# Optimization experiments

Hardware: AMD Instinct MI355X
Metric: run time of the kernel (lower is better)

The kernel has to match this reference:

```python
import jax, jax.numpy as jnp
import numpy as np

B, S0, DE, DT = 32, 255, 768, 256
D = DE + DT          # graph RNN input size
H = 512              # hidden_graph == hidden_edge (required by h_prev[0] = graph_state)
T = 256              # tag_representation_dim
M = 25


def _rnn_layer(x, Wih, Whh, bih, bhh):
    """Vanilla tanh RNN layer, batch_first. x: [B,S,Din] -> [B,S,H]."""
    xW = jnp.einsum('bsd,hd->bsh', x, Wih) + bih  # big GEMM hoisted out of scan
    h0 = jnp.zeros((x.shape[0], Whh.shape[0]), x.dtype)

    def step(h, xw):
        h = jnp.tanh(xw + h @ Whh.T + bhh)
        return h, h

    _, ys = jax.lax.scan(step, h0, jnp.swapaxes(xW, 0, 1))
    return jnp.swapaxes(ys, 0, 1)


def setup_inputs() -> dict:
    key = jax.random.key(0)
    ks = iter(jax.random.split(key, 40))

    def rn(shape, s=1.0):
        return jax.random.normal(next(ks), shape, jnp.float32) * s

    w = 0.04  # ~ uniform(-1/sqrt(H), 1/sqrt(H)) scale of torch RNN init
    return {
        'input': rn((B, S0, DE)),
        'tag_embeddings': rn((B, S0, DT)),
        'mask': jnp.ones((B, S0), jnp.int32),
        'sentinel': rn((D,)),
        'g0_Wih': rn((H, D), w), 'g0_Whh': rn((H, H), w), 'g0_bih': rn((H,), w), 'g0_bhh': rn((H,), w),
        'g1_Wih': rn((H, H), w), 'g1_Whh': rn((H, H), w), 'g1_bih': rn((H,), w), 'g1_bhh': rn((H,), w),
        'e0_Wih': rn((H, 1), w), 'e0_Whh': rn((H, H), w), 'e0_bih': rn((H,), w), 'e0_bhh': rn((H,), w),
        'e1_Wih': rn((H, H), w), 'e1_Whh': rn((H, H), w), 'e1_bih': rn((H,), w), 'e1_bhh': rn((H,), w),
        'cls_W': rn((1, H), w), 'cls_b': rn((1,), w),
        'ht_W': rn((T, H), w), 'ht_b': rn((T,), w),
        'dt_W': rn((T, H), w), 'dt_b': rn((T,), w),
    }


def reference(input, tag_embeddings, mask, sentinel,
              g0_Wih, g0_Whh, g0_bih, g0_bhh,
              g1_Wih, g1_Whh, g1_bih, g1_bhh,
              e0_Wih, e0_Whh, e0_bih, e0_bhh,
              e1_Wih, e1_Whh, e1_bih, e1_bhh,
              cls_W, cls_b, ht_W, ht_b, dt_W, dt_b):
    Bq = input.shape[0]
    x = jnp.concatenate([input, tag_embeddings], axis=-1)              # [B,S0,D]
    sent = jnp.broadcast_to(sentinel[None, None, :], (Bq, 1, x.shape[-1]))
    x = jnp.concatenate([sent, x], axis=1)                             # [B,S,D]
    S = x.shape[1]
    m = jnp.concatenate([jnp.ones((Bq, 1), mask.dtype), mask], axis=1)  # sentinel mask

    # --- graph RNN (2-layer tanh RNN); zero padded outputs == pad_packed_sequence ---
    y = _rnn_layer(x, g0_Wih, g0_Whh, g0_bih, g0_bhh)
    y = _rnn_layer(y, g1_Wih, g1_Whh, g1_bih, g1_bhh)
    graph_state = y * m[..., None].astype(y.dtype)                     # [B,S,H]

    N = Bq * S
    gs = graph_state.reshape(N, -1)        # layer-0 initial hidden
    x0 = jnp.ones((N, 1), graph_state.dtype)
    h1_0 = jnp.zeros_like(gs)              # layer-1 initial hidden

    def step(carry, _):
        xe, h0, h1 = carry
        h0 = jnp.tanh(xe @ e0_Wih.T + e0_bih + h0 @ e0_Whh.T + e0_bhh)
        h1 = jnp.tanh(h0 @ e1_Wih.T + e1_bih + h1 @ e1_Whh.T + e1_bhh)
        pred = h1 @ cls_W.T + cls_b        # [N,1]
        return (pred, h0, h1), pred

    _, preds = jax.lax.scan(step, (x0, gs, h1_0), None, length=M)      # [M,N,1]
    A = jnp.concatenate([x0[:, None, :], jnp.swapaxes(preds, 0, 1)], axis=1)[..., 0]  # [N,M+1]

    # --- reshape_adj: banded GraphRNN predictions -> square adjacency logits ---
    A3 = A.reshape(Bq, S, M + 1)
    i = jnp.arange(S)[:, None]
    j = jnp.arange(S)[None, :]
    k = i - j                                # offset of node j behind node i
    valid = (k >= 0) & (k <= M)
    rows = jnp.broadcast_to(i, (S, S))
    arc = A3[:, rows, jnp.clip(k, 0, M)]     # [B,S,S]
    arc_logits = jnp.where(valid[None], arc, jnp.zeros((), arc.dtype))

    # --- tag heads (dropout is identity at eval) ---
    head_tag = jax.nn.elu(graph_state @ ht_W.T + ht_b)
    dep_tag = jax.nn.elu(graph_state @ dt_W.T + dt_b)
    return arc_logits, head_tag, dep_tag
```

## Files before the change

### kernel.cpp

```cpp
#include <hip/hip_runtime.h>
#include <math.h>

typedef unsigned int u32;
typedef unsigned short u16;
typedef unsigned long long u64;
typedef __attribute__((ext_vector_type(8))) short short8;
typedef __attribute__((ext_vector_type(4))) float f32x4;

__device__ inline float bf2f(u16 v) { return __uint_as_float(((u32)v) << 16); }
__device__ inline u16 f2bf(float f) {
  u32 u = __float_as_uint(f);
  return (u16)((u + 0x7fffu + ((u >> 16) & 1u)) >> 16);
}
__device__ inline float fast_tanh(float x) {
  x = fminf(9.0f, fmaxf(-9.0f, x));
  float e = __builtin_amdgcn_exp2f(x * 2.8853900817779268f);
  return (e - 1.0f) * __builtin_amdgcn_rcpf(e + 1.0f);
}
__device__ inline void gload16(const void* g, void* l) {
  __builtin_amdgcn_global_load_lds((const __attribute__((address_space(1))) u32*)g,
                                   (__attribute__((address_space(3))) u32*)l, 16, 0, 0);
}

__global__ void k_transw(float* __restrict__ outp, const float* __restrict__ src) {
  int idx = blockIdx.x * 256 + threadIdx.x;
  int k = idx & 511, t = idx >> 9;
  outp[(size_t)k * 512 + t] = src[(size_t)t * 512 + k];
}

__global__ void k_split(u16* __restrict__ hi, u16* __restrict__ lo,
                        const float* __restrict__ src, int n) {
  int i = blockIdx.x * 256 + threadIdx.x;
  if (i >= n) return;
  float v = src[i];
  u16 h = f2bf(v);
  hi[i] = h;
  lo[i] = f2bf(v - bf2f(h));
}

__global__ void k_concat_split(u16* __restrict__ xhi, u16* __restrict__ xlo,
                               const float* __restrict__ inp, const float* __restrict__ tag,
                               const float* __restrict__ sent) {
  int gid = blockIdx.x * 256 + threadIdx.x;
  int row = gid >> 10, c = gid & 1023;
  int b = row >> 8, s = row & 255;
  float v;
  if (s == 0) v = sent[c];
  else if (c < 768) v = inp[(size_t)(b * 255 + s - 1) * 768 + c];
  else v = tag[(size_t)(b * 255 + s - 1) * 256 + (c - 768)];
  u16 h = f2bf(v);
  xhi[gid] = h;
  xlo[gid] = f2bf(v - bf2f(h));
}

__global__ void k_syncinit(u64* hbuf) {
  int i = blockIdx.x * 256 + threadIdx.x;
  if (i < 32768) {
    int pos = i & 1023;
    hbuf[i] = (pos < 512) ? (1ull << 32) : 0ull;
  }
}

__global__ __launch_bounds__(512, 1) void k_gscan_mb(
    float* __restrict__ XW, const float* __restrict__ WT,
    const int* __restrict__ mask, int layer, u64* hbuf)
{
  __shared__ float hls[528];
  const int blk = blockIdx.x;
  const int b = blk >> 2, q = blk & 3;
  const int tid = threadIdx.x;
  const int lane = tid & 63;
  const int wv = tid >> 6;
  const int colL = wv * 16 + (lane & 15);
  const int p = (lane >> 4) & 3;
  const int c = (q << 7) + colL;
  const bool fin = (p == 0);
  float wreg[128];
#pragma unroll
  for (int i = 0; i < 128; ++i)
    wreg[i] = WT[(size_t)(p * 128 + i) * 512 + c];
  u64* hb = hbuf + b * 1024;
  __syncthreads();

  for (int s = 0; s < 256; ++s) {
    float xwv = 0.f;
    size_t xwoff = 0;
    if (fin) {
      xwoff = (size_t)(b * 256 + s) * 512 + c;
      xwv = XW[xwoff];
    }
    const u32 want = (u32)(s + 1);
    u64 v;
    do {
      v = __hip_atomic_load(&hb[(s & 1) * 512 + tid], __ATOMIC_RELAXED,
                            __HIP_MEMORY_SCOPE_AGENT);
    } while ((u32)(v >> 32) < want);
    hls[(tid >> 7) * 132 + (tid & 127)] = __uint_as_float((u32)v);
    __syncthreads();
    const float* hk = &hls[p * 132];
    float a0 = 0.f, a1 = 0.f, a2 = 0.f, a3 = 0.f;
#pragma unroll
    for (int i = 0; i < 128; i += 4) {
      a0 = fmaf(wreg[i],     hk[i],     a0);
      a1 = fmaf(wreg[i + 1], hk[i + 1], a1);
      a2 = fmaf(wreg[i + 2], hk[i + 2], a2);
      a3 = fmaf(wreg[i + 3], hk[i + 3], a3);
    }
    float r = (a0 + a1) + (a2 + a3);
    r += __shfl_xor(r, 16);
    r += __shfl_xor(r, 32);
    if (fin) {
      float h = tanhf(r + xwv);
      u64 pk = ((u64)(u32)(s + 2) << 32) | (u64)__float_as_uint(h);
      __hip_atomic_store(&hb[((s + 1) & 1) * 512 + c], pk,
                         __ATOMIC_RELAXED, __HIP_MEMORY_SCOPE_AGENT);
      float ov = h;
      if (layer) ov *= (s == 0) ? 1.f : (float)mask[b * 255 + s - 1];
      XW[xwoff] = ov;
    }
    __syncthreads();
  }
}

__global__ void k_cvt(u16* __restrict__ dst, const float* __restrict__ src) {
  int i = blockIdx.x * 256 + threadIdx.x;
  dst[i] = f2bf(src[i]);
}
__global__ void k_zero(uint4* p) {
  p[(size_t)blockIdx.x * 256 + threadIdx.x] = uint4{0u, 0u, 0u, 0u};
}

__device__ inline void tile_map(int blk, int& m0, int& n0) {
  n0 = (blk >> 6) << 6;
  m0 = (blk & 63) << 7;
}

template<int KD>
__global__ __launch_bounds__(256, 2) void gemm_s(
    const u16* __restrict__ Ahi, const u16* __restrict__ Alo,
    const u16* __restrict__ Whi, const u16* __restrict__ Wlo,
    const float* __restrict__ b1, const float* __restrict__ b2,
    float* __restrict__ outf)
{
  __shared__ __attribute__((aligned(16))) u16 Ah[128 * 64];
  __shared__ __attribute__((aligned(16))) u16 Al[128 * 64];
  __shared__ __attribute__((aligned(16))) u16 Wh[64 * 64];
  __shared__ __attribute__((aligned(16))) u16 Wl[64 * 64];
  const int tid = threadIdx.x;
  const int lane = tid & 63, wid = tid >> 6;
  const int wr = wid >> 1, wc = wid & 1;
  int m0, n0;
  tile_map(blockIdx.x, m0, n0);
  const int rsub = lane >> 3;
  const int swz = (((lane & 7) ^ rsub) << 3);

  f32x4 zero4 = {0.f, 0.f, 0.f, 0.f};
  f32x4 acc[4][2];
#pragma unroll
  for (int i = 0; i < 4; ++i)
#pragma unroll
    for (int j = 0; j < 2; ++j) acc[i][j] = zero4;

  for (int kt = 0; kt < KD / 64; ++kt) {
    __syncthreads();
#pragma unroll
    for (int cc = 0; cc < 4; ++cc) {
      int row = wid * 32 + cc * 8 + rsub;
      size_t g = (size_t)(m0 + row) * KD + kt * 64 + swz;
      gload16(Ahi + g, &Ah[(wid * 32 + cc * 8) * 64]);
      gload16(Alo + g, &Al[(wid * 32 + cc * 8) * 64]);
    }
#pragma unroll
    for (int cc = 0; cc < 2; ++cc) {
      int row = wid * 16 + cc * 8 + rsub;
      size_t g = (size_t)(n0 + row) * KD + kt * 64 + swz;
      gload16(Whi + g, &Wh[(wid * 16 + cc * 8) * 64]);
      gload16(Wlo + g, &Wl[(wid * 16 + cc * 8) * 64]);
    }
    __syncthreads();
#pragma unroll
    for (int ks = 0; ks < 2; ++ks) {
      short8 ah[4], al[4], wh[2], wl[2];
#pragma unroll
      for (int mm = 0; mm < 4; ++mm) {
        int row = wr * 64 + mm * 16 + (lane & 15);
        int kb = (ks * 64 + ((lane >> 4) << 4)) ^ ((row & 7) << 4);
        ah[mm] = *(const short8*)((const char*)Ah + row * 128 + kb);
        al[mm] = *(const short8*)((const char*)Al + row * 128 + kb);
      }
#pragma unroll
      for (int nn = 0; nn < 2; ++nn) {
        int row = wc * 32 + nn * 16 + (lane & 15);
        int kb = (ks * 64 + ((lane >> 4) << 4)) ^ ((row & 7) << 4);
        wh[nn] = *(const short8*)((const char*)Wh + row * 128 + kb);
        wl[nn] = *(const short8*)((const char*)Wl + row * 128 + kb);
      }
#pragma unroll
      for (int mm = 0; mm < 4; ++mm)
#pragma unroll
        for (int nn = 0; nn < 2; ++nn) {
          acc[mm][nn] = __builtin_amdgcn_mfma_f32_16x16x32_bf16(ah[mm], wh[nn], acc[mm][nn], 0, 0, 0);
          acc[mm][nn] = __builtin_amdgcn_mfma_f32_16x16x32_bf16(ah[mm], wl[nn], acc[mm][nn], 0, 0, 0);
          acc[mm][nn] = __builtin_amdgcn_mfma_f32_16x16x32_bf16(al[mm], wh[nn], acc[mm][nn], 0, 0, 0);
        }
    }
  }

  float bcol[2];
#pragma unroll
  for (int nn = 0; nn < 2; ++nn) {
    int col = n0 + wc * 32 + nn * 16 + (lane & 15);
    bcol[nn] = b1[col] + b2[col];
  }
#pragma unroll
  for (int mm = 0; mm < 4; ++mm)
#pragma unroll
    for (int r = 0; r < 4; ++r) {
      int grow = m0 + wr * 64 + mm * 16 + ((lane >> 4) << 2) + r;
#pragma unroll
      for (int nn = 0; nn < 2; ++nn) {
        int col = n0 + wc * 32 + nn * 16 + (lane & 15);
        outf[(size_t)grow * 512 + col] = acc[mm][nn][r] + bcol[nn];
      }
    }
}

template<int MODE, int KD>
__global__ __launch_bounds__(256, 2) void gemm_k(
    const u16* __restrict__ Ag, const u16* __restrict__ Ag2,
    const u16* __restrict__ Wg, const u16* __restrict__ W2g,
    const float* __restrict__ b1, const float* __restrict__ b2,
    u16* __restrict__ outb, float* __restrict__ outh, float* __restrict__ outd,
    float* __restrict__ abuf, const float* __restrict__ vecw, int estep)
{
  __shared__ __attribute__((aligned(16))) u16 As[128 * 64];
  __shared__ __attribute__((aligned(16))) u16 Ws[64 * 64];
  __shared__ float xes[128];
  const int tid = threadIdx.x;
  const int lane = tid & 63, wid = tid >> 6;
  const int wr = wid >> 1, wc = wid & 1;
  int m0, n0;
  tile_map(blockIdx.x, m0, n0);
  const int rsub = lane >> 3;
  const int swz = (((lane & 7) ^ rsub) << 3);

  if constexpr (MODE == 2) {
    if (tid < 128) xes[tid] = abuf[(size_t)(m0 + tid) * 26 + estep];
  }

  f32x4 zero4 = {0.f, 0.f, 0.f, 0.f};
  f32x4 acc[4][2];
#pragma unroll
  for (int i = 0; i < 4; ++i)
#pragma unroll
    for (int j = 0; j < 2; ++j) acc[i][j] = zero4;

  for (int kt = 0; kt < KD / 64; ++kt) {
    const u16* Asrc; int ka;
    if (kt < 8) { Asrc = Ag;  ka = kt; }
    else        { Asrc = Ag2; ka = kt - 8; }
    const u16* Wsrc; int kw, rowoff;
    if constexpr (MODE == 1) {
      if (n0 >= 256) { Wsrc = W2g; rowoff = n0 - 256; }
      else           { Wsrc = Wg;  rowoff = n0; }
      kw = kt;
    } else {
      if (kt < 8) { Wsrc = Wg;  kw = kt; }
      else        { Wsrc = W2g; kw = kt - 8; }
      rowoff = n0;
    }
    __syncthreads();
#pragma unroll
    for (int cc = 0; cc < 4; ++cc) {
      int row = wid * 32 + cc * 8 + rsub;
      gload16(Asrc + (size_t)(m0 + row) * 512 + ka * 64 + swz, &As[(wid * 32 + cc * 8) * 64]);
    }
#pragma unroll
    for (int cc = 0; cc < 2; ++cc) {
      int row = wid * 16 + cc * 8 + rsub;
      gload16(Wsrc + (size_t)(rowoff + row) * 512 + kw * 64 + swz, &Ws[(wid * 16 + cc * 8) * 64]);
    }
    __syncthreads();
#pragma unroll
    for (int ks = 0; ks < 2; ++ks) {
      short8 af[4], bfv[2];
#pragma unroll
      for (int mm = 0; mm < 4; ++mm) {
        int row = wr * 64 + mm * 16 + (lane & 15);
        int kb = (ks * 64 + ((lane >> 4) << 4)) ^ ((row & 7) << 4);
        af[mm] = *(const short8*)((const char*)As + row * 128 + kb);
      }
#pragma unroll
      for (int nn = 0; nn < 2; ++nn) {
        int row = wc * 32 + nn * 16 + (lane & 15);
        int kb = (ks * 64 + ((lane >> 4) << 4)) ^ ((row & 7) << 4);
        bfv[nn] = *(const short8*)((const char*)Ws + row * 128 + kb);
      }
#pragma unroll
      for (int mm = 0; mm < 4; ++mm)
#pragma unroll
        for (int nn = 0; nn < 2; ++nn)
          acc[mm][nn] = __builtin_amdgcn_mfma_f32_16x16x32_bf16(af[mm], bfv[nn], acc[mm][nn], 0, 0, 0);
    }
  }

  float bcol[2], vcol[2];
#pragma unroll
  for (int nn = 0; nn < 2; ++nn) {
    int col = n0 + wc * 32 + nn * 16 + (lane & 15);
    if constexpr (MODE == 1) bcol[nn] = (col < 256) ? b1[col] : b2[col - 256];
    else                     bcol[nn] = b1[col] + b2[col];
    vcol[nn] = 0.0f;
    if constexpr (MODE == 2 || MODE == 3) vcol[nn] = vecw[col];
  }
  float pp[4][4];
#pragma unroll
  for (int i = 0; i < 4; ++i)
#pragma unroll
    for (int j = 0; j < 4; ++j) pp[i][j] = 0.0f;

#pragma unroll
  for (int mm = 0; mm < 4; ++mm) {
#pragma unroll
    for (int r = 0; r < 4; ++r) {
      int lrow = wr * 64 + mm * 16 + ((lane >> 4) << 2) + r;
      int grow = m0 + lrow;
#pragma unroll
      for (int nn = 0; nn < 2; ++nn) {
        int col = n0 + wc * 32 + nn * 16 + (lane & 15);
        float v = acc[mm][nn][r] + bcol[nn];
        if constexpr (MODE == 1) {
          float e = v > 0.f ? v : (expf(v) - 1.f);
          if (col < 256) outh[(size_t)grow * 256 + col] = e;
          else           outd[(size_t)grow * 256 + (col - 256)] = e;
        } else if constexpr (MODE == 2) {
          v += xes[lrow] * vcol[nn];
          outb[(size_t)grow * 512 + col] = f2bf(fast_tanh(v));
        } else {
          float h = fast_tanh(v);
          outb[(size_t)grow * 512 + col] = f2bf(h);
          pp[mm][r] += h * vcol[nn];
        }
      }
    }
  }
  if constexpr (MODE == 3) {
#pragma unroll
    for (int mm = 0; mm < 4; ++mm)
#pragma unroll
      for (int r = 0; r < 4; ++r) {
        float p = pp[mm][r];
        p += __shfl_xor(p, 1); p += __shfl_xor(p, 2);
        p += __shfl_xor(p, 4); p += __shfl_xor(p, 8);
        if ((lane & 15) == 0) {
          int grow = m0 + wr * 64 + mm * 16 + ((lane >> 4) << 2) + r;
          atomicAdd(&abuf[(size_t)grow * 26 + estep + 1], p);
        }
      }
  }
}

__global__ void k_ainit(float* abuf, const float* clsb) {
  int idx = blockIdx.x * 256 + threadIdx.x;
  if (idx >= 212992) return;
  abuf[idx] = ((idx % 26) == 0) ? 1.0f : clsb[0];
}
__global__ void k_arc(float* __restrict__ outp, const float* __restrict__ abuf) {
  int idx = blockIdx.x * 256 + threadIdx.x;
  int j = idx & 255, i = (idx >> 8) & 255, b = idx >> 16;
  int k = i - j;
  outp[idx] = (k >= 0 && k <= 25) ? abuf[(size_t)(b * 256 + i) * 26 + k] : 0.0f;
}
__global__ void k_diag(float* __restrict__ outp, float code, int n) {
  int idx = blockIdx.x * 256 + threadIdx.x;
  if (idx < n) outp[idx] = (idx == 0) ? code : 0.0f;
}

extern "C" void kernel_launch(void* const* d_in, const int* in_sizes, int n_in,
                              void* d_out, int out_size, void* d_ws, size_t ws_size,
                              hipStream_t stream) {
  static const int SZ[26] = {6266880, 2088960, 8160, 1024, 524288, 262144, 512, 512,
                             262144, 262144, 512, 512, 512, 262144, 512, 512,
                             262144, 262144, 512, 512, 512, 1, 131072, 256, 131072, 256};
  float diag_code = 0.0f;
  if (n_in != 26) diag_code = 4096.0f + (float)n_in;
  else {
    for (int j = 0; j < 26; ++j)
      if (in_sizes[j] != SZ[j]) { diag_code = 2048.0f + (float)j; break; }
  }
  const size_t NEED = (size_t)(32u << 20);
  if (ws_size < NEED && diag_code == 0.0f) diag_code = 8192.0f;
  if (diag_code != 0.0f) {
    k_diag<<<(out_size + 255) / 256, 256, 0, stream>>>((float*)d_out, diag_code, out_size);
    return;
  }

  const float* inp  = (const float*)d_in[0];
  const float* tag  = (const float*)d_in[1];
  const int*   mask = (const int*)d_in[2];
  const float* sent = (const float*)d_in[3];
  const float* g0_Wih = (const float*)d_in[4];
  const float* g0_Whh = (const float*)d_in[5];
  const float* g0_bih = (const float*)d_in[6];
  const float* g0_bhh = (const float*)d_in[7];
  const float* g1_Wih = (const float*)d_in[8];
  const float* g1_Whh = (const float*)d_in[9];
  const float* g1_bih = (const float*)d_in[10];
  const float* g1_bhh = (const float*)d_in[11];
  const float* e0_Wih = (const float*)d_in[12];
  const float* e0_Whh = (const float*)d_in[13];
  const float* e0_bih = (const float*)d_in[14];
  const float* e0_bhh = (const float*)d_in[15];
  const float* e1_Wih = (const float*)d_in[16];
  const float* e1_Whh = (const float*)d_in[17];
  const float* e1_bih = (const float*)d_in[18];
  const float* e1_bhh = (const float*)d_in[19];
  const float* cls_W  = (const float*)d_in[20];
  const float* cls_b  = (const float*)d_in[21];
  const float* ht_W   = (const float*)d_in[22];
  const float* ht_b   = (const float*)d_in[23];
  const float* dt_W   = (const float*)d_in[24];
  const float* dt_b   = (const float*)d_in[25];

  float* out = (float*)d_out;
  char*  ob  = (char*)d_out;
  char*  ws  = (char*)d_ws;

  u16*  W0hi = (u16*)(ob);
  u16*  W0lo = (u16*)(ob + (1u << 20));
  float* XW0 = (float*)(ob + (2u << 20));
  float* WT0 = (float*)(ob + (18u << 20));
  float* WT1 = (float*)(ob + (19u << 20));
  u16*  G1hi = (u16*)(ob + (20u << 20));
  u16*  G1lo = (u16*)(ob + (20u << 20) + (512u << 10));
  u16*  Xhi  = (u16*)(ws);
  u16*  Xlo  = (u16*)(ws + (16u << 20));
  u16*  Y0hi = (u16*)(ws);
  u16*  Y0lo = (u16*)(ws + (8u << 20));
  u16*  S0   = Y0hi;
  u16*  S1   = Y0lo;
  u16*  S2   = (u16*)(ws + (16u << 20));
  float* ABUF = (float*)(ws + (24u << 20));
  u16*  W0b  = (u16*)(ws + (25u << 20));
  u16*  W1b  = (u16*)(ws + (25u << 20) + (512u << 10));
  u16*  W2b  = (u16*)(ws + (26u << 20));
  u16*  W3b  = (u16*)(ws + (26u << 20) + (512u << 10));
  u16*  W4b  = (u16*)(ws + (26u << 20) + (768u << 10));
  u64*  HBUF = (u64*)(ws + (28u << 20));

  k_concat_split<<<32768, 256, 0, stream>>>(Xhi, Xlo, inp, tag, sent);
  k_split<<<2048, 256, 0, stream>>>(W0hi, W0lo, g0_Wih, 524288);
  k_transw<<<1024, 256, 0, stream>>>(WT0, g0_Whh);
  k_transw<<<1024, 256, 0, stream>>>(WT1, g1_Whh);
  k_split<<<1024, 256, 0, stream>>>(G1hi, G1lo, g1_Wih, 262144);

  gemm_s<1024><<<512, 256, 0, stream>>>(Xhi, Xlo, W0hi, W0lo, g0_bih, g0_bhh, XW0);
  k_syncinit<<<128, 256, 0, stream>>>(HBUF);
  k_gscan_mb<<<128, 512, 0, stream>>>(XW0, WT0, mask, 0, HBUF);

  k_split<<<16384, 256, 0, stream>>>(Y0hi, Y0lo, XW0, 4194304);
  gemm_s<512><<<512, 256, 0, stream>>>(Y0hi, Y0lo, G1hi, G1lo, g1_bih, g1_bhh, XW0);
  k_syncinit<<<128, 256, 0, stream>>>(HBUF);
  k_gscan_mb<<<128, 512, 0, stream>>>(XW0, WT1, mask, 1, HBUF);

  k_cvt<<<16384, 256, 0, stream>>>(S0, XW0);
  k_zero<<<2048, 256, 0, stream>>>((uint4*)S1);
  k_cvt<<<1024, 256, 0, stream>>>(W0b, e0_Whh);
  k_cvt<<<1024, 256, 0, stream>>>(W1b, e1_Wih);
  k_cvt<<<1024, 256, 0, stream>>>(W2b, e1_Whh);
  k_cvt<<<512, 256, 0, stream>>>(W3b, ht_W);
  k_cvt<<<512, 256, 0, stream>>>(W4b, dt_W);

  gemm_k<1, 512><<<512, 256, 0, stream>>>(S0, nullptr, W3b, W4b, ht_b, dt_b,
                                          nullptr, out + 2097152, out + 4194304,
                                          nullptr, nullptr, 0);

  k_ainit<<<832, 256, 0, stream>>>(ABUF, cls_b);
  u16* r0 = S0; u16* r1 = S1; u16* r2 = S2;
  for (int st = 0; st < 25; ++st) {
    gemm_k<2, 512><<<512, 256, 0, stream>>>(r0, nullptr, W0b, nullptr, e0_bih, e0_bhh,
                                            r2, nullptr, nullptr, ABUF, e0_Wih, st);
    gemm_k<3, 1024><<<512, 256, 0, stream>>>(r2, r1, W1b, W2b, e1_bih, e1_bhh,
                                             r0, nullptr, nullptr, ABUF, cls_W, st);
    u16* t0 = r2; u16* t1 = r0; u16* t2 = r1;
    r0 = t0; r1 = t1; r2 = t2;
  }
  k_arc<<<8192, 256, 0, stream>>>(out, ABUF);
}
```

Before: 1.798 ms.

## Fuse prep kernels, emit bf16 from scan, widen GEMM tiles to 128x128

The many small preprocessing kernels (transposes, hi/lo splits, casts, sync-buffer init, zeroing, ABUF init) are merged into three multi-role launches. The recurrent scan kernel now writes its outputs directly as bf16, either as a hi/lo pair or as a masked single value, which removes the separate split and convert passes over the activations. It also double-buffers its shared hidden-state array so one __syncthreads per step can be dropped. The GEMM kernels move from 128x64 to 128x128 output tiles, halving the grid to 256 blocks to get more reuse per block, at the cost of more registers per thread and fewer concurrent blocks.

After: 1.668 ms. -7.2%, faster.

```diff
diff --git a/kernel.cpp b/kernel.cpp
--- a/kernel.cpp
+++ b/kernel.cpp
@@ -22,50 +22,100 @@
                                    (__attribute__((address_space(3))) u32*)l, 16, 0, 0);
 }
 
-__global__ void k_transw(float* __restrict__ outp, const float* __restrict__ src) {
-  int idx = blockIdx.x * 256 + threadIdx.x;
-  int k = idx & 511, t = idx >> 9;
-  outp[(size_t)k * 512 + t] = src[(size_t)t * 512 + k];
-}
-
-__global__ void k_split(u16* __restrict__ hi, u16* __restrict__ lo,
-                        const float* __restrict__ src, int n) {
-  int i = blockIdx.x * 256 + threadIdx.x;
-  if (i >= n) return;
-  float v = src[i];
-  u16 h = f2bf(v);
-  hi[i] = h;
-  lo[i] = f2bf(v - bf2f(h));
-}
-
-__global__ void k_concat_split(u16* __restrict__ xhi, u16* __restrict__ xlo,
-                               const float* __restrict__ inp, const float* __restrict__ tag,
-                               const float* __restrict__ sent) {
-  int gid = blockIdx.x * 256 + threadIdx.x;
-  int row = gid >> 10, c = gid & 1023;
-  int b = row >> 8, s = row & 255;
-  float v;
-  if (s == 0) v = sent[c];
-  else if (c < 768) v = inp[(size_t)(b * 255 + s - 1) * 768 + c];
-  else v = tag[(size_t)(b * 255 + s - 1) * 256 + (c - 768)];
-  u16 h = f2bf(v);
-  xhi[gid] = h;
-  xlo[gid] = f2bf(v - bf2f(h));
-}
-
-__global__ void k_syncinit(u64* hbuf) {
-  int i = blockIdx.x * 256 + threadIdx.x;
-  if (i < 32768) {
+__device__ inline void tile_map(int blk, int& m0, int& n0) {
+  n0 = (blk >> 6) << 7;
+  m0 = (blk & 63) << 7;
+}
+
+__global__ void k_prep1(u16* __restrict__ xhi, u16* __restrict__ xlo,
+                        const float* __restrict__ inp, const float* __restrict__ tag,
+                        const float* __restrict__ sent,
+                        u16* __restrict__ w0hi, u16* __restrict__ w0lo,
+                        const float* __restrict__ g0wih,
+                        float* __restrict__ wt0, const float* __restrict__ g0whh,
+                        float* __restrict__ wt1, const float* __restrict__ g1whh,
+                        u16* __restrict__ g1hi, u16* __restrict__ g1lo,
+                        const float* __restrict__ g1wih) {
+  int blk = blockIdx.x, t = threadIdx.x;
+  if (blk < 32768) {
+    int gid = blk * 256 + t;
+    int row = gid >> 10, c = gid & 1023;
+    int b = row >> 8, s = row & 255;
+    float v;
+    if (s == 0) v = sent[c];
+    else if (c < 768) v = inp[(size_t)(b * 255 + s - 1) * 768 + c];
+    else v = tag[(size_t)(b * 255 + s - 1) * 256 + (c - 768)];
+    u16 h = f2bf(v);
+    xhi[gid] = h;
+    xlo[gid] = f2bf(v - bf2f(h));
+  } else if (blk < 34816) {
+    int i = (blk - 32768) * 256 + t;
+    float v = g0wih[i];
+    u16 h = f2bf(v);
+    w0hi[i] = h;
+    w0lo[i] = f2bf(v - bf2f(h));
+  } else if (blk < 35840) {
+    int i = (blk - 34816) * 256 + t;
+    int k = i & 511, tt = i >> 9;
+    wt0[(size_t)k * 512 + tt] = g0whh[(size_t)tt * 512 + k];
+  } else if (blk < 36864) {
+    int i = (blk - 35840) * 256 + t;
+    int k = i & 511, tt = i >> 9;
+    wt1[(size_t)k * 512 + tt] = g1whh[(size_t)tt * 512 + k];
+  } else {
+    int i = (blk - 36864) * 256 + t;
+    float v = g1wih[i];
+    u16 h = f2bf(v);
+    g1hi[i] = h;
+    g1lo[i] = f2bf(v - bf2f(h));
+  }
+}
+
+__global__ void k_prep2(u64* __restrict__ hbuf,
+                        u16* __restrict__ w0b, const float* __restrict__ e0whh,
+                        u16* __restrict__ w1b, const float* __restrict__ e1wih,
+                        u16* __restrict__ w2b, const float* __restrict__ e1whh,
+                        u16* __restrict__ w3b, const float* __restrict__ htw,
+                        u16* __restrict__ w4b, const float* __restrict__ dtw,
+                        float* __restrict__ abuf, const float* __restrict__ clsb) {
+  int blk = blockIdx.x, t = threadIdx.x;
+  if (blk < 128) {
+    int i = blk * 256 + t;
     int pos = i & 1023;
     hbuf[i] = (pos < 512) ? (1ull << 32) : 0ull;
+  } else if (blk < 1152) {
+    int i = (blk - 128) * 256 + t;  w0b[i] = f2bf(e0whh[i]);
+  } else if (blk < 2176) {
+    int i = (blk - 1152) * 256 + t; w1b[i] = f2bf(e1wih[i]);
+  } else if (blk < 3200) {
+    int i = (blk - 2176) * 256 + t; w2b[i] = f2bf(e1whh[i]);
+  } else if (blk < 3712) {
+    int i = (blk - 3200) * 256 + t; w3b[i] = f2bf(htw[i]);
+  } else if (blk < 4224) {
+    int i = (blk - 3712) * 256 + t; w4b[i] = f2bf(dtw[i]);
+  } else {
+    int i = (blk - 4224) * 256 + t;
+    if (i < 212992) abuf[i] = ((i % 26) == 0) ? 1.0f : clsb[0];
+  }
+}
+
+__global__ void k_prep3(u64* __restrict__ hbuf, uint4* __restrict__ s1) {
+  int blk = blockIdx.x, t = threadIdx.x;
+  if (blk < 128) {
+    int i = blk * 256 + t;
+    int pos = i & 1023;
+    hbuf[i] = (pos < 512) ? (1ull << 32) : 0ull;
+  } else {
+    s1[(size_t)(blk - 128) * 256 + t] = uint4{0u, 0u, 0u, 0u};
   }
 }
 
 __global__ __launch_bounds__(512, 1) void k_gscan_mb(
-    float* __restrict__ XW, const float* __restrict__ WT,
-    const int* __restrict__ mask, int layer, u64* hbuf)
+    const float* __restrict__ XW, const float* __restrict__ WT,
+    const int* __restrict__ mask, int layer, u64* hbuf,
+    u16* __restrict__ o16a, u16* __restrict__ o16b)
 {
-  __shared__ float hls[528];
+  __shared__ float hls[2][528];
   const int blk = blockIdx.x;
   const int b = blk >> 2, q = blk & 3;
   const int tid = threadIdx.x;
@@ -80,14 +130,13 @@
   for (int i = 0; i < 128; ++i)
     wreg[i] = WT[(size_t)(p * 128 + i) * 512 + c];
   u64* hb = hbuf + b * 1024;
-  __syncthreads();
 
   for (int s = 0; s < 256; ++s) {
     float xwv = 0.f;
-    size_t xwoff = 0;
+    size_t off = 0;
     if (fin) {
-      xwoff = (size_t)(b * 256 + s) * 512 + c;
-      xwv = XW[xwoff];
+      off = (size_t)(b * 256 + s) * 512 + c;
+      xwv = XW[off];
     }
     const u32 want = (u32)(s + 1);
     u64 v;
@@ -95,9 +144,9 @@
       v = __hip_atomic_load(&hb[(s & 1) * 512 + tid], __ATOMIC_RELAXED,
                             __HIP_MEMORY_SCOPE_AGENT);
     } while ((u32)(v >> 32) < want);
-    hls[(tid >> 7) * 132 + (tid & 127)] = __uint_as_float((u32)v);
+    hls[s & 1][(tid >> 7) * 132 + (tid & 127)] = __uint_as_float((u32)v);
     __syncthreads();
-    const float* hk = &hls[p * 132];
+    const float* hk = &hls[s & 1][p * 132];
     float a0 = 0.f, a1 = 0.f, a2 = 0.f, a3 = 0.f;
 #pragma unroll
     for (int i = 0; i < 128; i += 4) {
@@ -114,25 +163,16 @@
       u64 pk = ((u64)(u32)(s + 2) << 32) | (u64)__float_as_uint(h);
       __hip_atomic_store(&hb[((s + 1) & 1) * 512 + c], pk,
                          __ATOMIC_RELAXED, __HIP_MEMORY_SCOPE_AGENT);
-      float ov = h;
-      if (layer) ov *= (s == 0) ? 1.f : (float)mask[b * 255 + s - 1];
-      XW[xwoff] = ov;
-    }
-    __syncthreads();
-  }
-}
-
-__global__ void k_cvt(u16* __restrict__ dst, const float* __restrict__ src) {
-  int i = blockIdx.x * 256 + threadIdx.x;
-  dst[i] = f2bf(src[i]);
-}
-__global__ void k_zero(uint4* p) {
-  p[(size_t)blockIdx.x * 256 + threadIdx.x] = uint4{0u, 0u, 0u, 0u};
-}
-
-__device__ inline void tile_map(int blk, int& m0, int& n0) {
-  n0 = (blk >> 6) << 6;
-  m0 = (blk & 63) << 7;
+      if (layer) {
+        float mv = (s == 0) ? 1.f : (float)mask[b * 255 + s - 1];
+        o16a[off] = f2bf(h * mv);
+      } else {
+        u16 hi = f2bf(h);
+        o16a[off] = hi;
+        o16b[off] = f2bf(h - bf2f(hi));
+      }
+    }
+  }
 }
 
 template<int KD>
@@ -144,8 +184,8 @@
 {
   __shared__ __attribute__((aligned(16))) u16 Ah[128 * 64];
   __shared__ __attribute__((aligned(16))) u16 Al[128 * 64];
-  __shared__ __attribute__((aligned(16))) u16 Wh[64 * 64];
-  __shared__ __attribute__((aligned(16))) u16 Wl[64 * 64];
+  __shared__ __attribute__((aligned(16))) u16 Wh[128 * 64];
+  __shared__ __attribute__((aligned(16))) u16 Wl[128 * 64];
   const int tid = threadIdx.x;
   const int lane = tid & 63, wid = tid >> 6;
   const int wr = wid >> 1, wc = wid & 1;
@@ -155,32 +195,28 @@
   const int swz = (((lane & 7) ^ rsub) << 3);
 
   f32x4 zero4 = {0.f, 0.f, 0.f, 0.f};
-  f32x4 acc[4][2];
+  f32x4 acc[4][4];
 #pragma unroll
   for (int i = 0; i < 4; ++i)
 #pragma unroll
-    for (int j = 0; j < 2; ++j) acc[i][j] = zero4;
+    for (int j = 0; j < 4; ++j) acc[i][j] = zero4;
 
   for (int kt = 0; kt < KD / 64; ++kt) {
     __syncthreads();
 #pragma unroll
     for (int cc = 0; cc < 4; ++cc) {
       int row = wid * 32 + cc * 8 + rsub;
-      size_t g = (size_t)(m0 + row) * KD + kt * 64 + swz;
-      gload16(Ahi + g, &Ah[(wid * 32 + cc * 8) * 64]);
-      gload16(Alo + g, &Al[(wid * 32 + cc * 8) * 64]);
-    }
-#pragma unroll
-    for (int cc = 0; cc < 2; ++cc) {
-      int row = wid * 16 + cc * 8 + rsub;
-      size_t g = (size_t)(n0 + row) * KD + kt * 64 + swz;
-      gload16(Whi + g, &Wh[(wid * 16 + cc * 8) * 64]);
-      gload16(Wlo + g, &Wl[(wid * 16 + cc * 8) * 64]);
+      size_t ga = (size_t)(m0 + row) * KD + kt * 64 + swz;
+      size_t gw = (size_t)(n0 + row) * KD + kt * 64 + swz;
+      gload16(Ahi + ga, &Ah[(wid * 32 + cc * 8) * 64]);
+      gload16(Alo + ga, &Al[(wid * 32 + cc * 8) * 64]);
+      gload16(Whi + gw, &Wh[(wid * 32 + cc * 8) * 64]);
+      gload16(Wlo + gw, &Wl[(wid * 32 + cc * 8) * 64]);
     }
     __syncthreads();
 #pragma unroll
     for (int ks = 0; ks < 2; ++ks) {
-      short8 ah[4], al[4], wh[2], wl[2];
+      short8 ah[4], al[4], wh[4], wl[4];
 #pragma unroll
       for (int mm = 0; mm < 4; ++mm) {
         int row = wr * 64 + mm * 16 + (lane & 15);
@@ -189,8 +225,8 @@
         al[mm] = *(const short8*)((const char*)Al + row * 128 + kb);
       }
 #pragma unroll
-      for (int nn = 0; nn < 2; ++nn) {
-        int row = wc * 32 + nn * 16 + (lane & 15);
+      for (int nn = 0; nn < 4; ++nn) {
+        int row = wc * 64 + nn * 16 + (lane & 15);
         int kb = (ks * 64 + ((lane >> 4) << 4)) ^ ((row & 7) << 4);
         wh[nn] = *(const short8*)((const char*)Wh + row * 128 + kb);
         wl[nn] = *(const short8*)((const char*)Wl + row * 128 + kb);
@@ -198,7 +234,7 @@
 #pragma unroll
       for (int mm = 0; mm < 4; ++mm)
 #pragma unroll
-        for (int nn = 0; nn < 2; ++nn) {
+        for (int nn = 0; nn < 4; ++nn) {
           acc[mm][nn] = __builtin_amdgcn_mfma_f32_16x16x32_bf16(ah[mm], wh[nn], acc[mm][nn], 0, 0, 0);
           acc[mm][nn] = __builtin_amdgcn_mfma_f32_16x16x32_bf16(ah[mm], wl[nn], acc[mm][nn], 0, 0, 0);
           acc[mm][nn] = __builtin_amdgcn_mfma_f32_16x16x32_bf16(al[mm], wh[nn], acc[mm][nn], 0, 0, 0);
@@ -206,10 +242,10 @@
     }
   }
 
-  float bcol[2];
-#pragma unroll
-  for (int nn = 0; nn < 2; ++nn) {
-    int col = n0 + wc * 32 + nn * 16 + (lane & 15);
+  float bcol[4];
+#pragma unroll
+  for (int nn = 0; nn < 4; ++nn) {
+    int col = n0 + wc * 64 + nn * 16 + (lane & 15);
     bcol[nn] = b1[col] + b2[col];
   }
 #pragma unroll
@@ -218,8 +254,8 @@
     for (int r = 0; r < 4; ++r) {
       int grow = m0 + wr * 64 + mm * 16 + ((lane >> 4) << 2) + r;
 #pragma unroll
-      for (int nn = 0; nn < 2; ++nn) {
-        int col = n0 + wc * 32 + nn * 16 + (lane & 15);
+      for (int nn = 0; nn < 4; ++nn) {
+        int col = n0 + wc * 64 + nn * 16 + (lane & 15);
         outf[(size_t)grow * 512 + col] = acc[mm][nn][r] + bcol[nn];
       }
     }
@@ -234,7 +270,7 @@
     float* __restrict__ abuf, const float* __restrict__ vecw, int estep)
 {
   __shared__ __attribute__((aligned(16))) u16 As[128 * 64];
-  __shared__ __attribute__((aligned(16))) u16 Ws[64 * 64];
+  __shared__ __attribute__((aligned(16))) u16 Ws[128 * 64];
   __shared__ float xes[128];
   const int tid = threadIdx.x;
   const int lane = tid & 63, wid = tid >> 6;
@@ -249,11 +285,11 @@
   }
 
   f32x4 zero4 = {0.f, 0.f, 0.f, 0.f};
-  f32x4 acc[4][2];
+  f32x4 acc[4][4];
 #pragma unroll
   for (int i = 0; i < 4; ++i)
 #pragma unroll
-    for (int j = 0; j < 2; ++j) acc[i][j] = zero4;
+    for (int j = 0; j < 4; ++j) acc[i][j] = zero4;
 
   for (int kt = 0; kt < KD / 64; ++kt) {
     const u16* Asrc; int ka;
@@ -274,16 +310,12 @@
     for (int cc = 0; cc < 4; ++cc) {
       int row = wid * 32 + cc * 8 + rsub;
       gload16(Asrc + (size_t)(m0 + row) * 512 + ka * 64 + swz, &As[(wid * 32 + cc * 8) * 64]);
-    }
-#pragma unroll
-    for (int cc = 0; cc < 2; ++cc) {
-      int row = wid * 16 + cc * 8 + rsub;
-      gload16(Wsrc + (size_t)(rowoff + row) * 512 + kw * 64 + swz, &Ws[(wid * 16 + cc * 8) * 64]);
+      gload16(Wsrc + (size_t)(rowoff + row) * 512 + kw * 64 + swz, &Ws[(wid * 32 + cc * 8) * 64]);
     }
     __syncthreads();
 #pragma unroll
     for (int ks = 0; ks < 2; ++ks) {
-      short8 af[4], bfv[2];
+      short8 af[4], wf[4];
 #pragma unroll
       for (int mm = 0; mm < 4; ++mm) {
         int row = wr * 64 + mm * 16 + (lane & 15);
@@ -291,23 +323,23 @@
         af[mm] = *(const short8*)((const char*)As + row * 128 + kb);
       }
 #pragma unroll
-      for (int nn = 0; nn < 2; ++nn) {
-        int row = wc * 32 + nn * 16 + (lane & 15);
+      for (int nn = 0; nn < 4; ++nn) {
+        int row = wc * 64 + nn * 16 + (lane & 15);
         int kb = (ks * 64 + ((lane >> 4) << 4)) ^ ((row & 7) << 4);
-        bfv[nn] = *(const short8*)((const char*)Ws + row * 128 + kb);
+        wf[nn] = *(const short8*)((const char*)Ws + row * 128 + kb);
       }
 #pragma unroll
       for (int mm = 0; mm < 4; ++mm)
 #pragma unroll
-        for (int nn = 0; nn < 2; ++nn)
-          acc[mm][nn] = __builtin_amdgcn_mfma_f32_16x16x32_bf16(af[mm], bfv[nn], acc[mm][nn], 0, 0, 0);
-    }
-  }
-
-  float bcol[2], vcol[2];
-#pragma unroll
-  for (int nn = 0; nn < 2; ++nn) {
-    int col = n0 + wc * 32 + nn * 16 + (lane & 15);
+        for (int nn = 0; nn < 4; ++nn)
+          acc[mm][nn] = __builtin_amdgcn_mfma_f32_16x16x32_bf16(af[mm], wf[nn], acc[mm][nn], 0, 0, 0);
+    }
+  }
+
+  float bcol[4], vcol[4];
+#pragma unroll
+  for (int nn = 0; nn < 4; ++nn) {
+    int col = n0 + wc * 64 + nn * 16 + (lane & 15);
     if constexpr (MODE == 1) bcol[nn] = (col < 256) ? b1[col] : b2[col - 256];
     else                     bcol[nn] = b1[col] + b2[col];
     vcol[nn] = 0.0f;
@@ -326,8 +358,8 @@
       int lrow = wr * 64 + mm * 16 + ((lane >> 4) << 2) + r;
       int grow = m0 + lrow;
 #pragma unroll
-      for (int nn = 0; nn < 2; ++nn) {
-        int col = n0 + wc * 32 + nn * 16 + (lane & 15);
+      for (int nn = 0; nn < 4; ++nn) {
+        int col = n0 + wc * 64 + nn * 16 + (lane & 15);
         float v = acc[mm][nn][r] + bcol[nn];
         if constexpr (MODE == 1) {
           float e = v > 0.f ? v : (expf(v) - 1.f);
@@ -360,11 +392,6 @@
   }
 }
 
-__global__ void k_ainit(float* abuf, const float* clsb) {
-  int idx = blockIdx.x * 256 + threadIdx.x;
-  if (idx >= 212992) return;
-  abuf[idx] = ((idx % 26) == 0) ? 1.0f : clsb[0];
-}
 __global__ void k_arc(float* __restrict__ outp, const float* __restrict__ abuf) {
   int idx = blockIdx.x * 256 + threadIdx.x;
   int j = idx & 255, i = (idx >> 8) & 255, b = idx >> 16;
@@ -448,39 +475,24 @@
   u16*  W4b  = (u16*)(ws + (26u << 20) + (768u << 10));
   u64*  HBUF = (u64*)(ws + (28u << 20));
 
-  k_concat_split<<<32768, 256, 0, stream>>>(Xhi, Xlo, inp, tag, sent);
-  k_split<<<2048, 256, 0, stream>>>(W0hi, W0lo, g0_Wih, 524288);
-  k_transw<<<1024, 256, 0, stream>>>(WT0, g0_Whh);
-  k_transw<<<1024, 256, 0, stream>>>(WT1, g1_Whh);
-  k_split<<<1024, 256, 0, stream>>>(G1hi, G1lo, g1_Wih, 262144);
-
-  gemm_s<1024><<<512, 256, 0, stream>>>(Xhi, Xlo, W0hi, W0lo, g0_bih, g0_bhh, XW0);
-  k_syncinit<<<128, 256, 0, stream>>>(HBUF);
-  k_gscan_mb<<<128, 512, 0, stream>>>(XW0, WT0, mask, 0, HBUF);
-
-  k_split<<<16384, 256, 0, stream>>>(Y0hi, Y0lo, XW0, 4194304);
-  gemm_s<512><<<512, 256, 0, stream>>>(Y0hi, Y0lo, G1hi, G1lo, g1_bih, g1_bhh, XW0);
-  k_syncinit<<<128, 256, 0, stream>>>(HBUF);
-  k_gscan_mb<<<128, 512, 0, stream>>>(XW0, WT1, mask, 1, HBUF);
-
-  k_cvt<<<16384, 256, 0, stream>>>(S0, XW0);
-  k_zero<<<2048, 256, 0, stream>>>((uint4*)S1);
-  k_cvt<<<1024, 256, 0, stream>>>(W0b, e0_Whh);
-  k_cvt<<<1024, 256, 0, stream>>>(W1b, e1_Wih);
-  k_cvt<<<1024, 256, 0, stream>>>(W2b, e1_Whh);
-  k_cvt<<<512, 256, 0, stream>>>(W3b, ht_W);
-  k_cvt<<<512, 256, 0, stream>>>(W4b, dt_W);
-
-  gemm_k<1, 512><<<512, 256, 0, stream>>>(S0, nullptr, W3b, W4b, ht_b, dt_b,
+  k_prep1<<<37888, 256, 0, stream>>>(Xhi, Xlo, inp, tag, sent,
+                                     W0hi, W0lo, g0_Wih, WT0, g0_Whh, WT1, g1_Whh,
+                                     G1hi, G1lo, g1_Wih);
+  gemm_s<1024><<<256, 256, 0, stream>>>(Xhi, Xlo, W0hi, W0lo, g0_bih, g0_bhh, XW0);
+  k_prep2<<<5056, 256, 0, stream>>>(HBUF, W0b, e0_Whh, W1b, e1_Wih, W2b, e1_Whh,
+                                    W3b, ht_W, W4b, dt_W, ABUF, cls_b);
+  k_gscan_mb<<<128, 512, 0, stream>>>(XW0, WT0, mask, 0, HBUF, Y0hi, Y0lo);
+  gemm_s<512><<<256, 256, 0, stream>>>(Y0hi, Y0lo, G1hi, G1lo, g1_bih, g1_bhh, XW0);
+  k_prep3<<<2176, 256, 0, stream>>>(HBUF, (uint4*)S1);
+  k_gscan_mb<<<128, 512, 0, stream>>>(XW0, WT1, mask, 1, HBUF, S0, nullptr);
+  gemm_k<1, 512><<<256, 256, 0, stream>>>(S0, nullptr, W3b, W4b, ht_b, dt_b,
                                           nullptr, out + 2097152, out + 4194304,
                                           nullptr, nullptr, 0);
-
-  k_ainit<<<832, 256, 0, stream>>>(ABUF, cls_b);
   u16* r0 = S0; u16* r1 = S1; u16* r2 = S2;
   for (int st = 0; st < 25; ++st) {
-    gemm_k<2, 512><<<512, 256, 0, stream>>>(r0, nullptr, W0b, nullptr, e0_bih, e0_bhh,
+    gemm_k<2, 512><<<256, 256, 0, stream>>>(r0, nullptr, W0b, nullptr, e0_bih, e0_bhh,
                                             r2, nullptr, nullptr, ABUF, e0_Wih, st);
-    gemm_k<3, 1024><<<512, 256, 0, stream>>>(r2, r1, W1b, W2b, e1_bih, e1_bhh,
+    gemm_k<3, 1024><<<256, 256, 0, stream>>>(r2, r1, W1b, W2b, e1_bih, e1_bhh,
                                              r0, nullptr, nullptr, ABUF, cls_W, st);
     u16* t0 = r2; u16* t1 = r0; u16* t2 = r1;
     r0 = t0; r1 = t1; r2 = t2;
```
